# Performance work log

Measured on AMD Instinct MI355X. Metric: run time of the kernel, lower is better.

The kernel has to match this reference:

```python
import jax, jax.numpy as jnp
import numpy as np

N_NODES = 50000
N_EDGES = 600000
D_IN = 128
D_OUT = 128


def setup_inputs() -> dict:
    key = jax.random.key(0)
    ks = jax.random.split(key, 10)
    feat = jax.random.normal(ks[0], (N_NODES, D_IN), dtype=jnp.float32)
    src = jax.random.randint(ks[1], (N_EDGES,), 0, N_NODES, dtype=jnp.int32)
    dst = jax.random.randint(ks[2], (N_EDGES,), 0, N_NODES, dtype=jnp.int32)
    node_type = jax.random.randint(ks[3], (N_NODES,), 0, 2) > 0  # bool: True=cell
    # Xavier-uniform with relu gain, as in reset_parameters
    gain = float(np.sqrt(2.0))
    lim = gain * float(np.sqrt(6.0 / (D_IN + D_OUT)))
    W_self = jax.random.uniform(ks[4], (D_OUT, D_IN), jnp.float32, -lim, lim)
    b_self = jnp.zeros((D_OUT,), jnp.float32)
    W_neigh = jax.random.uniform(ks[5], (D_OUT, D_IN), jnp.float32, -lim, lim)
    b_neigh = jnp.zeros((D_OUT,), jnp.float32)
    w_cell = jnp.array([1.0], jnp.float32)
    w_gene = jnp.array([1.0], jnp.float32)
    return {"feat": feat, "W_self": W_self, "b_self": b_self,
            "W_neigh": W_neigh, "b_neigh": b_neigh,
            "w_cell": w_cell, "w_gene": w_gene,
            "src": src, "dst": dst, "node_type": node_type}


def reference(feat, W_self, b_self, W_neigh, b_neigh, w_cell, w_gene, src, dst, node_type):
    # mean aggregation over incoming edges: neigh[v] = mean_{(u->v)} feat[u]
    msg_sum = jax.ops.segment_sum(feat[src], dst, num_segments=N_NODES)  # [N, D_IN]
    deg = jax.ops.segment_sum(jnp.ones_like(dst, dtype=feat.dtype), dst,
                              num_segments=N_NODES)  # [N]
    h_neigh = msg_sum / jnp.maximum(deg, 1.0)[:, None]  # zero-degree nodes -> 0
    # per-node self weight by node type (cell vs gene)
    self_w = jnp.where(node_type[:, None], w_cell[0], w_gene[0])  # [N,1]
    rst = self_w * (feat @ W_self.T + b_self) + (h_neigh @ W_neigh.T + b_neigh)
    return rst
```

## Files before the change

kernel.cpp:

```cpp
#include <hip/hip_runtime.h>

#define N_NODES 50000
#define N_EDGES 600000
#define D 128
#define SCAN_BLK 512
#define SCAN_NBLK ((N_NODES + SCAN_BLK - 1) / SCAN_BLK)
#define GNB 64

typedef __attribute__((ext_vector_type(8))) short bf16x8;
typedef __attribute__((ext_vector_type(4))) float f32x4;

static __device__ __forceinline__ unsigned short f2bf(float f) {
    unsigned u = __float_as_uint(f);
    unsigned r = (u + 0x7FFFu + ((u >> 16) & 1u)) >> 16;
    return (unsigned short)r;
}
static __device__ __forceinline__ float bf2f(unsigned short b) {
    return __uint_as_float(((unsigned)b) << 16);
}

__global__ __launch_bounds__(256)
void convF(const float* __restrict__ in, unsigned short* __restrict__ out) {
    const int i = blockIdx.x * 256 + threadIdx.x;
    const float4 v = ((const float4*)in)[i];
    ushort4 o;
    o.x = f2bf(v.x); o.y = f2bf(v.y); o.z = f2bf(v.z); o.w = f2bf(v.w);
    ((ushort4*)out)[i] = o;
}

__global__ __launch_bounds__(256)
void convW(const float* __restrict__ Ws, const float* __restrict__ Wn,
           unsigned short* __restrict__ Wsb, unsigned short* __restrict__ Wnb) {
    const int i = blockIdx.x * 256 + threadIdx.x;
    if (i < D * D) Wsb[i] = f2bf(Ws[i]);
    else           Wnb[i - D * D] = f2bf(Wn[i - D * D]);
}

__global__ __launch_bounds__(256)
void hist_deg(const int* __restrict__ dst, int* __restrict__ deg) {
    const int e = blockIdx.x * 256 + threadIdx.x;
    if (e < N_EDGES) atomicAdd(&deg[dst[e]], 1);
}

__global__ __launch_bounds__(SCAN_BLK)
void scanA(const int* __restrict__ deg, int* __restrict__ rowptr,
           int* __restrict__ bsum) {
    __shared__ int tmp[SCAN_BLK];
    const int t = threadIdx.x;
    const int i = blockIdx.x * SCAN_BLK + t;
    tmp[t] = (i < N_NODES) ? deg[i] : 0;
    __syncthreads();
    for (int off = 1; off < SCAN_BLK; off <<= 1) {
        int x = (t >= off) ? tmp[t - off] : 0;
        __syncthreads();
        tmp[t] += x;
        __syncthreads();
    }
    if (i < N_NODES) rowptr[1 + i] = tmp[t];
    if (t == SCAN_BLK - 1) bsum[blockIdx.x] = tmp[t];
}

__global__ void scanB(const int* __restrict__ bsum, int* __restrict__ bofs,
                      int* __restrict__ rowptr) {
    if (threadIdx.x == 0) {
        int run = 0;
        for (int b = 0; b < SCAN_NBLK; ++b) { bofs[b] = run; run += bsum[b]; }
        rowptr[0] = 0;
    }
}

__global__ __launch_bounds__(SCAN_BLK)
void scanC(int* __restrict__ rowptr, const int* __restrict__ bofs) {
    const int i = blockIdx.x * SCAN_BLK + threadIdx.x;
    if (i < N_NODES) rowptr[1 + i] += bofs[blockIdx.x];
}

__global__ __launch_bounds__(256)
void fill_csr(const int* __restrict__ src, const int* __restrict__ dst,
              const int* __restrict__ rowptr, int* __restrict__ cursor,
              int* __restrict__ col) {
    const int e = blockIdx.x * 256 + threadIdx.x;
    if (e >= N_EDGES) return;
    const int d = dst[e];
    const int p = atomicAdd(&cursor[d], 1);
    col[rowptr[d] + p] = src[e];
}

__global__ __launch_bounds__(256)
void gather_mean(const unsigned short* __restrict__ fb,
                 const int* __restrict__ rowptr, const int* __restrict__ col,
                 unsigned short* __restrict__ hb) {
    const int wid = (blockIdx.x * 256 + threadIdx.x) >> 6;
    const int lane = threadIdx.x & 63;
    if (wid >= N_NODES) return;
    const int beg = rowptr[wid], end = rowptr[wid + 1];
    float ax = 0.f, ay = 0.f;
    int i = beg;
    for (; i + 3 < end; i += 4) {
        const int s0 = col[i], s1 = col[i + 1], s2 = col[i + 2], s3 = col[i + 3];
        const unsigned u0 = *(const unsigned*)(fb + (size_t)s0 * D + lane * 2);
        const unsigned u1 = *(const unsigned*)(fb + (size_t)s1 * D + lane * 2);
        const unsigned u2 = *(const unsigned*)(fb + (size_t)s2 * D + lane * 2);
        const unsigned u3 = *(const unsigned*)(fb + (size_t)s3 * D + lane * 2);
        ax += bf2f((unsigned short)u0) + bf2f((unsigned short)u1)
            + bf2f((unsigned short)u2) + bf2f((unsigned short)u3);
        ay += bf2f((unsigned short)(u0 >> 16)) + bf2f((unsigned short)(u1 >> 16))
            + bf2f((unsigned short)(u2 >> 16)) + bf2f((unsigned short)(u3 >> 16));
    }
    for (; i < end; ++i) {
        const unsigned u = *(const unsigned*)(fb + (size_t)col[i] * D + lane * 2);
        ax += bf2f((unsigned short)u);
        ay += bf2f((unsigned short)(u >> 16));
    }
    const float rs = 1.f / fmaxf((float)(end - beg), 1.f);
    const unsigned o = (unsigned)f2bf(ax * rs) | ((unsigned)f2bf(ay * rs) << 16);
    *(unsigned*)(hb + (size_t)wid * D + lane * 2) = o;
}

__global__ __launch_bounds__(256)
void fused_gemm(const unsigned short* __restrict__ fb,
                const unsigned short* __restrict__ hb,
                const unsigned short* __restrict__ Wsb,
                const unsigned short* __restrict__ Wnb,
                const float* __restrict__ bs, const float* __restrict__ bn,
                const unsigned char* __restrict__ ntype,
                const float* __restrict__ w_cell, const float* __restrict__ w_gene,
                float* __restrict__ out) {
    const int t = threadIdx.x;
    const int w = t >> 6, l = t & 63;
    const int lr = l & 15;
    const int kb = (l >> 4) * 8;
    const int arow = blockIdx.x * GNB + w * 16 + lr;
    const size_t arowc = (size_t)min(arow, N_NODES - 1);

    f32x4 accS[8], accN[8];
#pragma unroll
    for (int j = 0; j < 8; ++j) {
        accS[j] = (f32x4){0.f, 0.f, 0.f, 0.f};
        accN[j] = (f32x4){0.f, 0.f, 0.f, 0.f};
    }

#pragma unroll
    for (int ks = 0; ks < 4; ++ks) {
        const int ko = ks * 32 + kb;
        const bf16x8 aS = *(const bf16x8*)(fb + arowc * D + ko);
        const bf16x8 aN = *(const bf16x8*)(hb + arowc * D + ko);
#pragma unroll
        for (int j = 0; j < 8; ++j) {
            const bf16x8 bS = *(const bf16x8*)(Wsb + (size_t)(j * 16 + lr) * D + ko);
            const bf16x8 bN = *(const bf16x8*)(Wnb + (size_t)(j * 16 + lr) * D + ko);
            accS[j] = __builtin_amdgcn_mfma_f32_16x16x32_bf16(aS, bS, accS[j], 0, 0, 0);
            accN[j] = __builtin_amdgcn_mfma_f32_16x16x32_bf16(aN, bN, accN[j], 0, 0, 0);
        }
    }

    const int drow0 = blockIdx.x * GNB + w * 16 + (l >> 4) * 4;
#pragma unroll
    for (int r = 0; r < 4; ++r) {
        const int v = drow0 + r;
        if (v < N_NODES) {
            const float sw = ntype[v] ? w_cell[0] : w_gene[0];
#pragma unroll
            for (int j = 0; j < 8; ++j) {
                const int c = j * 16 + lr;
                out[(size_t)v * D + c] = sw * (accS[j][r] + bs[c]) + accN[j][r] + bn[c];
            }
        }
    }
}

extern "C" void kernel_launch(void* const* d_in, const int* in_sizes, int n_in,
                              void* d_out, int out_size, void* d_ws, size_t ws_size,
                              hipStream_t stream) {
    const float* feat   = (const float*)d_in[0];
    const float* W_self = (const float*)d_in[1];
    const float* b_self = (const float*)d_in[2];
    const float* W_nei  = (const float*)d_in[3];
    const float* b_nei  = (const float*)d_in[4];
    const float* w_cell = (const float*)d_in[5];
    const float* w_gene = (const float*)d_in[6];
    const int*   src    = (const int*)d_in[7];
    const int*   dst    = (const int*)d_in[8];
    const unsigned char* ntype = (const unsigned char*)d_in[9];
    float* out = (float*)d_out;

    unsigned short* fb  = (unsigned short*)d_ws;
    unsigned short* hb  = fb + (size_t)N_NODES * D;
    unsigned short* Wsb = hb + (size_t)N_NODES * D;
    unsigned short* Wnb = Wsb + D * D;
    int* rowptr = (int*)(Wnb + D * D);
    int* deg    = rowptr + N_NODES + 4;
    int* cursor = deg + N_NODES;
    int* bsum   = cursor + N_NODES;
    int* bofs   = bsum + 128;
    int* col    = bofs + 128;

    hipMemsetAsync(deg, 0, 2 * N_NODES * sizeof(int), stream);

    convF<<<(N_NODES * D / 4) / 256, 256, 0, stream>>>(feat, fb);
    convW<<<(2 * D * D) / 256, 256, 0, stream>>>(W_self, W_nei, Wsb, Wnb);

    hist_deg<<<(N_EDGES + 255) / 256, 256, 0, stream>>>(dst, deg);
    scanA<<<SCAN_NBLK, SCAN_BLK, 0, stream>>>(deg, rowptr, bsum);
    scanB<<<1, 64, 0, stream>>>(bsum, bofs, rowptr);
    scanC<<<SCAN_NBLK, SCAN_BLK, 0, stream>>>(rowptr, bofs);
    fill_csr<<<(N_EDGES + 255) / 256, 256, 0, stream>>>(src, dst, rowptr, cursor, col);

    gather_mean<<<(N_NODES * 64 + 255) / 256, 256, 0, stream>>>(fb, rowptr, col, hb);

    fused_gemm<<<(N_NODES + GNB - 1) / GNB, 256, 0, stream>>>(
        fb, hb, Wsb, Wnb, b_self, b_nei, ntype, w_cell, w_gene, out);
}
```

Measured before the change: 233.0 us.

## Fuse prep kernels, single-block rowptr scan, deeper gather unroll

Merges the feature/weight bf16 conversion, degree histogram and cursor zeroing into one prep kernel. The three-kernel scan is replaced by a single 1024-thread block that scans 49 entries per thread serially. The gather loop is unrolled to 8 edges to keep more loads in flight. The aim is fewer launches and less launch latency. The cost is that the single-block scan does strided, uncoalesced per-thread reads and runs on one CU.

```diff
diff --git a/kernel.cpp b/kernel.cpp
--- a/kernel.cpp
+++ b/kernel.cpp
@@ -3,9 +3,8 @@
 #define N_NODES 50000
 #define N_EDGES 600000
 #define D 128
-#define SCAN_BLK 512
-#define SCAN_NBLK ((N_NODES + SCAN_BLK - 1) / SCAN_BLK)
 #define GNB 64
+#define NPT 49
 
 typedef __attribute__((ext_vector_type(8))) short bf16x8;
 typedef __attribute__((ext_vector_type(4))) float f32x4;
@@ -20,59 +19,60 @@
 }
 
 __global__ __launch_bounds__(256)
-void convF(const float* __restrict__ in, unsigned short* __restrict__ out) {
-    const int i = blockIdx.x * 256 + threadIdx.x;
-    const float4 v = ((const float4*)in)[i];
-    ushort4 o;
-    o.x = f2bf(v.x); o.y = f2bf(v.y); o.z = f2bf(v.z); o.w = f2bf(v.w);
-    ((ushort4*)out)[i] = o;
-}
-
-__global__ __launch_bounds__(256)
-void convW(const float* __restrict__ Ws, const float* __restrict__ Wn,
-           unsigned short* __restrict__ Wsb, unsigned short* __restrict__ Wnb) {
-    const int i = blockIdx.x * 256 + threadIdx.x;
-    if (i < D * D) Wsb[i] = f2bf(Ws[i]);
-    else           Wnb[i - D * D] = f2bf(Wn[i - D * D]);
-}
-
-__global__ __launch_bounds__(256)
-void hist_deg(const int* __restrict__ dst, int* __restrict__ deg) {
-    const int e = blockIdx.x * 256 + threadIdx.x;
-    if (e < N_EDGES) atomicAdd(&deg[dst[e]], 1);
-}
-
-__global__ __launch_bounds__(SCAN_BLK)
-void scanA(const int* __restrict__ deg, int* __restrict__ rowptr,
-           int* __restrict__ bsum) {
-    __shared__ int tmp[SCAN_BLK];
+void prep(const float* __restrict__ feat, unsigned short* __restrict__ fb,
+          const float* __restrict__ Ws, const float* __restrict__ Wn,
+          unsigned short* __restrict__ Wsb, unsigned short* __restrict__ Wnb,
+          const int* __restrict__ dst, int* __restrict__ deg,
+          int* __restrict__ cursor) {
+    const int gid = blockIdx.x * 256 + threadIdx.x;
+    {
+        const float4 v = ((const float4*)feat)[gid];
+        ushort4 o;
+        o.x = f2bf(v.x); o.y = f2bf(v.y); o.z = f2bf(v.z); o.w = f2bf(v.w);
+        ((ushort4*)fb)[gid] = o;
+    }
+    if (gid < 2 * D * D / 4) {
+        const int half = D * D / 4;
+        const float4 v = (gid < half) ? ((const float4*)Ws)[gid]
+                                      : ((const float4*)Wn)[gid - half];
+        ushort4 o;
+        o.x = f2bf(v.x); o.y = f2bf(v.y); o.z = f2bf(v.z); o.w = f2bf(v.w);
+        if (gid < half) ((ushort4*)Wsb)[gid] = o;
+        else            ((ushort4*)Wnb)[gid - half] = o;
+    }
+    if (gid < N_EDGES) atomicAdd(&deg[dst[gid]], 1);
+    if (gid < N_NODES) cursor[gid] = 0;
+}
+
+__global__ __launch_bounds__(1024)
+void scan_rowptr(const int* __restrict__ deg, int* __restrict__ rowptr) {
+    __shared__ int part[1024];
     const int t = threadIdx.x;
-    const int i = blockIdx.x * SCAN_BLK + t;
-    tmp[t] = (i < N_NODES) ? deg[i] : 0;
+    const int i0 = t * NPT;
+    int local[NPT];
+    int s = 0;
+#pragma unroll
+    for (int k = 0; k < NPT; ++k) {
+        const int i = i0 + k;
+        const int d = (i < N_NODES) ? deg[i] : 0;
+        local[k] = s;
+        s += d;
+    }
+    part[t] = s;
     __syncthreads();
-    for (int off = 1; off < SCAN_BLK; off <<= 1) {
-        int x = (t >= off) ? tmp[t - off] : 0;
+    for (int off = 1; off < 1024; off <<= 1) {
+        const int x = (t >= off) ? part[t - off] : 0;
         __syncthreads();
-        tmp[t] += x;
+        part[t] += x;
         __syncthreads();
     }
-    if (i < N_NODES) rowptr[1 + i] = tmp[t];
-    if (t == SCAN_BLK - 1) bsum[blockIdx.x] = tmp[t];
-}
-
-__global__ void scanB(const int* __restrict__ bsum, int* __restrict__ bofs,
-                      int* __restrict__ rowptr) {
-    if (threadIdx.x == 0) {
-        int run = 0;
-        for (int b = 0; b < SCAN_NBLK; ++b) { bofs[b] = run; run += bsum[b]; }
-        rowptr[0] = 0;
-    }
-}
-
-__global__ __launch_bounds__(SCAN_BLK)
-void scanC(int* __restrict__ rowptr, const int* __restrict__ bofs) {
-    const int i = blockIdx.x * SCAN_BLK + threadIdx.x;
-    if (i < N_NODES) rowptr[1 + i] += bofs[blockIdx.x];
+    const int base = (t > 0) ? part[t - 1] : 0;
+#pragma unroll
+    for (int k = 0; k < NPT; ++k) {
+        const int i = i0 + k;
+        if (i < N_NODES) rowptr[i] = base + local[k];
+    }
+    if (t == 1023) rowptr[N_NODES] = part[1023];
 }
 
 __global__ __launch_bounds__(256)
@@ -96,16 +96,27 @@
     const int beg = rowptr[wid], end = rowptr[wid + 1];
     float ax = 0.f, ay = 0.f;
     int i = beg;
+    for (; i + 7 < end; i += 8) {
+        unsigned u[8];
+#pragma unroll
+        for (int q = 0; q < 8; ++q)
+            u[q] = *(const unsigned*)(fb + (size_t)col[i + q] * D + lane * 2);
+#pragma unroll
+        for (int q = 0; q < 8; ++q) {
+            ax += bf2f((unsigned short)u[q]);
+            ay += bf2f((unsigned short)(u[q] >> 16));
+        }
+    }
     for (; i + 3 < end; i += 4) {
-        const int s0 = col[i], s1 = col[i + 1], s2 = col[i + 2], s3 = col[i + 3];
-        const unsigned u0 = *(const unsigned*)(fb + (size_t)s0 * D + lane * 2);
-        const unsigned u1 = *(const unsigned*)(fb + (size_t)s1 * D + lane * 2);
-        const unsigned u2 = *(const unsigned*)(fb + (size_t)s2 * D + lane * 2);
-        const unsigned u3 = *(const unsigned*)(fb + (size_t)s3 * D + lane * 2);
-        ax += bf2f((unsigned short)u0) + bf2f((unsigned short)u1)
-            + bf2f((unsigned short)u2) + bf2f((unsigned short)u3);
-        ay += bf2f((unsigned short)(u0 >> 16)) + bf2f((unsigned short)(u1 >> 16))
-            + bf2f((unsigned short)(u2 >> 16)) + bf2f((unsigned short)(u3 >> 16));
+        unsigned u[4];
+#pragma unroll
+        for (int q = 0; q < 4; ++q)
+            u[q] = *(const unsigned*)(fb + (size_t)col[i + q] * D + lane * 2);
+#pragma unroll
+        for (int q = 0; q < 4; ++q) {
+            ax += bf2f((unsigned short)u[q]);
+            ay += bf2f((unsigned short)(u[q] >> 16));
+        }
     }
     for (; i < end; ++i) {
         const unsigned u = *(const unsigned*)(fb + (size_t)col[i] * D + lane * 2);
@@ -191,19 +202,15 @@
     int* rowptr = (int*)(Wnb + D * D);
     int* deg    = rowptr + N_NODES + 4;
     int* cursor = deg + N_NODES;
-    int* bsum   = cursor + N_NODES;
-    int* bofs   = bsum + 128;
-    int* col    = bofs + 128;
-
-    hipMemsetAsync(deg, 0, 2 * N_NODES * sizeof(int), stream);
-
-    convF<<<(N_NODES * D / 4) / 256, 256, 0, stream>>>(feat, fb);
-    convW<<<(2 * D * D) / 256, 256, 0, stream>>>(W_self, W_nei, Wsb, Wnb);
-
-    hist_deg<<<(N_EDGES + 255) / 256, 256, 0, stream>>>(dst, deg);
-    scanA<<<SCAN_NBLK, SCAN_BLK, 0, stream>>>(deg, rowptr, bsum);
-    scanB<<<1, 64, 0, stream>>>(bsum, bofs, rowptr);
-    scanC<<<SCAN_NBLK, SCAN_BLK, 0, stream>>>(rowptr, bofs);
+    int* col    = cursor + N_NODES;
+
+    hipMemsetAsync(deg, 0, N_NODES * sizeof(int), stream);
+
+    prep<<<(N_NODES * D / 4) / 256, 256, 0, stream>>>(
+        feat, fb, W_self, W_nei, Wsb, Wnb, dst, deg, cursor);
+
+    scan_rowptr<<<1, 1024, 0, stream>>>(deg, rowptr);
+
     fill_csr<<<(N_EDGES + 255) / 256, 256, 0, stream>>>(src, dst, rowptr, cursor, col);
 
     gather_mean<<<(N_NODES * 64 + 255) / 256, 256, 0, stream>>>(fb, rowptr, col, hb);
```

Result: slower. 267.6 us (+14.8%).
